# Kernel tuning notes

Measured on AMD Instinct MI355X. Metric: run time of the kernel, lower is better.

The kernel has to match this reference:

```python
import jax, jax.numpy as jnp
import numpy as np

D_MODEL = 1024
N_HEADS = 16  # long-term branch; short/medium use N_HEADS // 2


def _band_bias(seq_len, scale_factor):
    # Intended semantics of create_temporal_mask: position i may attend to
    # positions j >= i - scale_factor (recent past + all future); positions
    # further than scale_factor in the past are blocked.
    i = jnp.arange(seq_len)[:, None]
    j = jnp.arange(seq_len)[None, :]
    return jnp.where(j >= i - scale_factor, 0.0, -1e9).astype(jnp.float32)


def _mha(x, w_in, b_in, w_out, b_out, n_heads, bias):
    # Faithful nn.MultiheadAttention (batch_first, eval/no dropout).
    B, S, D = x.shape
    dk = D // n_heads
    qkv = x @ w_in.T + b_in                       # [B,S,3D]
    q, k, v = jnp.split(qkv, 3, axis=-1)
    def heads(t):
        return t.reshape(B, S, n_heads, dk).transpose(0, 2, 1, 3)  # [B,H,S,dk]
    q, k, v = heads(q), heads(k), heads(v)
    scores = jnp.einsum('bhid,bhjd->bhij', q, k) / np.sqrt(dk).astype(np.float32)
    if bias is not None:
        scores = scores + bias
    attn = jax.nn.softmax(scores, axis=-1)        # [B,H,S,S]
    out = jnp.einsum('bhij,bhjd->bhid', attn, v)  # [B,H,S,dk]
    out = out.transpose(0, 2, 1, 3).reshape(B, S, D)
    return out @ w_out.T + b_out, attn


def _layernorm(x, gamma, beta, eps=1e-5):
    mu = jnp.mean(x, axis=-1, keepdims=True)
    var = jnp.var(x, axis=-1, keepdims=True)
    return (x - mu) * jax.lax.rsqrt(var + eps) * gamma + beta


def setup_inputs() -> dict:
    key = jax.random.key(0)
    ks = jax.random.split(key, 12)
    D = D_MODEL
    s = 0.02
    inp = {
        'x': jax.random.normal(ks[0], (2, 2048, D), dtype=jnp.float32),
        'w_in_s': jax.random.normal(ks[1], (3 * D, D), dtype=jnp.float32) * s,
        'b_in_s': jnp.zeros((3 * D,), dtype=jnp.float32),
        'wo_s': jax.random.normal(ks[2], (D, D), dtype=jnp.float32) * s,
        'bo_s': jnp.zeros((D,), dtype=jnp.float32),
        'w_in_m': jax.random.normal(ks[3], (3 * D, D), dtype=jnp.float32) * s,
        'b_in_m': jnp.zeros((3 * D,), dtype=jnp.float32),
        'wo_m': jax.random.normal(ks[4], (D, D), dtype=jnp.float32) * s,
        'bo_m': jnp.zeros((D,), dtype=jnp.float32),
        'w_in_l': jax.random.normal(ks[5], (3 * D, D), dtype=jnp.float32) * s,
        'b_in_l': jnp.zeros((3 * D,), dtype=jnp.float32),
        'wo_l': jax.random.normal(ks[6], (D, D), dtype=jnp.float32) * s,
        'bo_l': jnp.zeros((D,), dtype=jnp.float32),
        'w_comb': jax.random.normal(ks[7], (D, 3 * D), dtype=jnp.float32) * s,
        'b_comb': jnp.zeros((D,), dtype=jnp.float32),
        'gamma': jnp.ones((D,), dtype=jnp.float32),
        'beta': jnp.zeros((D,), dtype=jnp.float32),
    }
    return inp


def reference(x, w_in_s, b_in_s, wo_s, bo_s,
              w_in_m, b_in_m, wo_m, bo_m,
              w_in_l, b_in_l, wo_l, bo_l,
              w_comb, b_comb, gamma, beta):
    B, S, D = x.shape
    short_bias = _band_bias(S, 10)
    medium_bias = _band_bias(S, 30)
    short_out, _ = _mha(x, w_in_s, b_in_s, wo_s, bo_s, N_HEADS // 2, short_bias)
    medium_out, _ = _mha(x, w_in_m, b_in_m, wo_m, bo_m, N_HEADS // 2, medium_bias)
    long_out, attn = _mha(x, w_in_l, b_in_l, wo_l, bo_l, N_HEADS, None)
    attn_weights = jnp.mean(attn, axis=1)  # torch default average_attn_weights=True -> [B,S,S]
    combined = jnp.concatenate([short_out, medium_out, long_out], axis=-1)
    output = combined @ w_comb.T + b_comb
    return _layernorm(output + x, gamma, beta), attn_weights
```

## Files before the change

kernel.cpp:

```cpp
#include <hip/hip_runtime.h>
#include <hip/hip_bf16.h>
#include <math.h>

#define B_ 2
#define S_ 2048
#define D_ 1024
#define M_ (B_*S_)
#define CTXLD 3072

typedef _Float16 half8_t __attribute__((ext_vector_type(8)));
typedef _Float16 half4_t __attribute__((ext_vector_type(4)));
typedef float    f32x4  __attribute__((ext_vector_type(4)));

#define GL2LDS(g, l) __builtin_amdgcn_global_load_lds( \
    (const __attribute__((address_space(1))) void*)(uintptr_t)(g), \
    (__attribute__((address_space(3))) void*)(l), 16, 0, 0)

struct GemmBatch {
    const _Float16* A;
    const _Float16* W;
    const float*    bias;
    void*           C;
    void*           C2;
};

template<int MODE>
__global__ __launch_bounds__(256) void gemm_f16(
    GemmBatch b0, GemmBatch b1, GemmBatch b2, int lda, int ldw, int ldc, int K)
{
    __shared__ __align__(16) _Float16 As[2*128*32];
    __shared__ __align__(16) _Float16 Bs[2*128*32];

    const GemmBatch G = (blockIdx.z == 0) ? b0 : ((blockIdx.z == 1) ? b1 : b2);

    const int t = threadIdx.x, lane = t & 63, w = t >> 6;
    const int bm = blockIdx.x * 128, bn = blockIdx.y * 128;
    const int wm = (w >> 1) * 64, wn = (w & 1) * 64;
    const int fr = lane & 15, q8 = (lane >> 4) * 8;
    const int srow = lane >> 2, scol = (lane & 3) * 8;

    f32x4 acc[4][4] = {};

    const _Float16* Ab = G.A + (size_t)(bm + w*32 + srow) * lda + scol;
    const _Float16* Wb = G.W + (size_t)(bn + w*32 + srow) * ldw + scol;

    for (int k0 = 0; k0 < K; k0 += 64) {
        __syncthreads();
        #pragma unroll
        for (int kc = 0; kc < 2; kc++)
            #pragma unroll
            for (int ii = 0; ii < 2; ii++) {
                GL2LDS(Ab + (size_t)(ii*16)*lda + k0 + kc*32,
                       As + kc*4096 + w*1024 + ii*512);
                GL2LDS(Wb + (size_t)(ii*16)*ldw + k0 + kc*32,
                       Bs + kc*4096 + w*1024 + ii*512);
            }
        __syncthreads();
        #pragma unroll
        for (int kc = 0; kc < 2; kc++) {
            half8_t af[4], bf[4];
            #pragma unroll
            for (int mt = 0; mt < 4; mt++)
                af[mt] = *(const half8_t*)&As[kc*4096 + (wm + mt*16 + fr)*32 + q8];
            #pragma unroll
            for (int nt = 0; nt < 4; nt++)
                bf[nt] = *(const half8_t*)&Bs[kc*4096 + (wn + nt*16 + fr)*32 + q8];
            #pragma unroll
            for (int mt = 0; mt < 4; mt++)
                #pragma unroll
                for (int nt = 0; nt < 4; nt++)
                    acc[mt][nt] = __builtin_amdgcn_mfma_f32_16x16x32_f16(
                        af[mt], bf[nt], acc[mt][nt], 0, 0, 0);
        }
    }

    const int cl = lane & 15;
    const int rq = (lane >> 4) * 4;

    if (MODE == 2 && bn >= 2048) {
        #pragma unroll
        for (int mt = 0; mt < 4; mt++) {
            int row0 = bm + wm + mt*16 + rq;
            #pragma unroll
            for (int nt = 0; nt < 4; nt++) {
                int gcol = bn + wn + nt*16 + cl;
                float bv = G.bias[gcol];
                half4_t hv = {(_Float16)(acc[mt][nt][0] + bv),
                              (_Float16)(acc[mt][nt][1] + bv),
                              (_Float16)(acc[mt][nt][2] + bv),
                              (_Float16)(acc[mt][nt][3] + bv)};
                *(half4_t*)((_Float16*)G.C2 + (size_t)(gcol - 2048) * M_ + row0) = hv;
            }
        }
        return;
    }

    #pragma unroll
    for (int mt = 0; mt < 4; mt++) {
        #pragma unroll
        for (int r = 0; r < 4; r++) {
            size_t grow = (size_t)(bm + wm + mt*16 + rq + r);
            #pragma unroll
            for (int nt = 0; nt < 4; nt++) {
                int gcol = bn + wn + nt*16 + cl;
                float v = acc[mt][nt][r] + ((MODE == 3) ? 0.f : G.bias[gcol]);
                if (MODE == 0)
                    ((float*)G.C)[grow * ldc + gcol] = v;
                else
                    ((_Float16*)G.C)[grow * ldc + gcol] = (_Float16)v;
            }
        }
    }
}

struct CastArgs {
    const float* s[5];
    _Float16*    d[5];
    int          nb[5];
};

__global__ __launch_bounds__(256) void cast_all(CastArgs a)
{
    int off = blockIdx.x;
    int seg = 0;
    while (seg < 4 && off >= a.nb[seg]) { off -= a.nb[seg]; seg++; }
    int i = off * 256 + threadIdx.x;
    float4 v = ((const float4*)a.s[seg])[i];
    half4_t h = {(_Float16)v.x, (_Float16)v.y, (_Float16)v.z, (_Float16)v.w};
    ((half4_t*)a.d[seg])[i] = h;
}

__global__ __launch_bounds__(256) void transpose_cast_wo(
    const float* s0, const float* s1, const float* s2,
    _Float16* d0, _Float16* d1, _Float16* d2)
{
    __shared__ float T[64][68];
    const float* src = blockIdx.z == 0 ? s0 : (blockIdx.z == 1 ? s1 : s2);
    _Float16*    dst = blockIdx.z == 0 ? d0 : (blockIdx.z == 1 ? d1 : d2);
    const int db = blockIdx.x * 64;
    const int eb = blockIdx.y * 64;
    const int r = threadIdx.x >> 4;
    const int c = (threadIdx.x & 15) * 4;

    #pragma unroll
    for (int rr = 0; rr < 4; rr++) {
        float4 v = *(const float4*)&src[(size_t)(db + rr*16 + r)*1024 + eb + c];
        T[rr*16 + r][c+0] = v.x; T[rr*16 + r][c+1] = v.y;
        T[rr*16 + r][c+2] = v.z; T[rr*16 + r][c+3] = v.w;
    }
    __syncthreads();
    #pragma unroll
    for (int rr = 0; rr < 4; rr++) {
        int e = rr*16 + r;
        half4_t hv = {(_Float16)T[c+0][e], (_Float16)T[c+1][e],
                      (_Float16)T[c+2][e], (_Float16)T[c+3][e]};
        *(half4_t*)&dst[(size_t)(eb + e)*1024 + db + c] = hv;
    }
}

__global__ __launch_bounds__(256) void beff_kernel(
    const float* __restrict__ w_comb, const float* __restrict__ b_comb,
    const float* __restrict__ bo_s, const float* __restrict__ bo_m,
    const float* __restrict__ bo_l, float* __restrict__ beff)
{
    __shared__ float red[4];
    const int n = blockIdx.x, t = threadIdx.x;
    float s = 0.f;
    for (int d = t; d < 1024; d += 256)
        s += w_comb[(size_t)n*3072 + d]        * bo_s[d]
           + w_comb[(size_t)n*3072 + 1024 + d] * bo_m[d]
           + w_comb[(size_t)n*3072 + 2048 + d] * bo_l[d];
    #pragma unroll
    for (int m = 32; m >= 1; m >>= 1) s += __shfl_xor(s, m);
    if ((t & 63) == 0) red[t >> 6] = s;
    __syncthreads();
    if (t == 0) beff[n] = b_comb[n] + red[0] + red[1] + red[2] + red[3];
}

template<int DK, int H, int NBR, bool LOUT>
__global__ __launch_bounds__(256, 4) void flash3(
    const _Float16* __restrict__ qk0, const _Float16* __restrict__ qk1,
    const _Float16* __restrict__ vT0, const _Float16* __restrict__ vT1,
    _Float16* __restrict__ ctx0, _Float16* __restrict__ ctx1,
    float* __restrict__ lout, int win0, int win1)
{
    constexpr int KS  = DK / 32;
    constexpr int DT  = DK / 16;
    constexpr int LDP = 40;

    __shared__ __align__(16) _Float16 Ks[KS * 64 * 32];
    __shared__ __align__(16) _Float16 Vs[2 * DK * 32];
    __shared__ __align__(16) _Float16 Ps[4 * 16 * LDP];
    __shared__ float Lw[64];

    const int t = threadIdx.x, lane = t & 63, w = t >> 6;
    const int fr = lane & 15, g = lane >> 4, k8 = g * 8;
    const int blkQ = blockIdx.x * 64;
    const int qlo  = blkQ + w * 16;
    const int h    = blockIdx.y;

    int br, b;
    if (NBR == 2) { br = blockIdx.z >> 1; b = blockIdx.z & 1; }
    else          { br = 0;               b = blockIdx.z;     }

    const _Float16* qk = br ? qk1 : qk0;
    const _Float16* vT = br ? vT1 : vT0;
    _Float16*      ctx = br ? ctx1 : ctx0;
    const int   window = br ? win1 : win0;

    const float sc = ((DK == 128) ? 0.08838834764831845f : 0.125f) * 1.44269504f;

    _Float16* PsW = Ps + w * 16 * LDP;
    const int srow = lane >> 2;
    const int scol = (lane & 3) * 8;

    half8_t qf[KS];
    #pragma unroll
    for (int kk = 0; kk < KS; kk++)
        qf[kk] = *(const half8_t*)&qk[(size_t)(b*S_ + qlo + fr)*2048 + h*DK + kk*32 + k8];

    f32x4 O[DT] = {};
    float lsum = 0.f;

    for (int j0 = 0; j0 < S_; j0 += 64) {
        if (window >= 0 && j0 + 63 < blkQ - window) continue;
        __syncthreads();

        #pragma unroll
        for (int kk = 0; kk < KS; kk++)
            GL2LDS(&qk[(size_t)(b*S_ + j0 + w*16 + srow)*2048 + 1024 + h*DK + kk*32 + scol],
                   &Ks[kk*2048 + w*512]);
        #pragma unroll
        for (int jc = 0; jc < 2; jc++)
            #pragma unroll
            for (int ii = 0; ii < DK/64; ii++)
                GL2LDS(&vT[(size_t)(h*DK + w*(DK/4) + ii*16 + srow)*M_
                           + b*S_ + j0 + jc*32 + scol],
                       &Vs[jc*DK*32 + w*(DK/4)*32 + ii*512]);
        __syncthreads();

        f32x4 st[4];
        #pragma unroll
        for (int jt = 0; jt < 4; jt++) {
            f32x4 s = {};
            #pragma unroll
            for (int kk = 0; kk < KS; kk++) {
                half8_t kf = *(const half8_t*)&Ks[kk*2048 + (jt*16 + fr)*32 + k8];
                s = __builtin_amdgcn_mfma_f32_16x16x32_f16(kf, qf[kk], s, 0, 0, 0);
            }
            st[jt] = s;
        }

        const bool full = (window < 0) || (j0 >= qlo + 15 - window);
        #pragma unroll
        for (int kc = 0; kc < 2; kc++) {
            #pragma unroll
            for (int jh = 0; jh < 2; jh++) {
                int jt = kc*2 + jh;
                float p[4];
                #pragma unroll
                for (int r = 0; r < 4; r++) {
                    float pv = exp2f(st[jt][r] * sc);
                    if (!full) {
                        int jg = j0 + jt*16 + g*4 + r;
                        if (jg < (qlo + fr) - window) pv = 0.f;
                    }
                    p[r] = pv;
                    lsum += pv;
                }
                half4_t ph = {(_Float16)p[0], (_Float16)p[1],
                              (_Float16)p[2], (_Float16)p[3]};
                *(half4_t*)&PsW[fr*LDP + jh*16 + g*4] = ph;
            }
            half8_t pf = *(const half8_t*)&PsW[fr*LDP + k8];
            #pragma unroll
            for (int dt = 0; dt < DT; dt++) {
                half8_t vf = *(const half8_t*)&Vs[kc*DK*32 + (dt*16 + fr)*32 + k8];
                O[dt] = __builtin_amdgcn_mfma_f32_16x16x32_f16(pf, vf, O[dt], 0, 0, 0);
            }
        }
    }

    lsum += __shfl_xor(lsum, 16);
    lsum += __shfl_xor(lsum, 32);
    if (g == 0) Lw[w*16 + fr] = lsum;
    float linv[4];
    #pragma unroll
    for (int r = 0; r < 4; r++)
        linv[r] = 1.f / Lw[w*16 + g*4 + r];

    if (LOUT && g == 0)
        lout[(size_t)(b*H + h)*S_ + qlo + fr] = lsum;

    #pragma unroll
    for (int r = 0; r < 4; r++) {
        _Float16* cp = ctx + (size_t)(b*S_ + qlo + g*4 + r)*CTXLD + h*DK;
        #pragma unroll
        for (int dt = 0; dt < DT; dt++)
            cp[dt*16 + fr] = (_Float16)(O[dt][r] * linv[r]);
    }
}

__global__ __launch_bounds__(256, 4) void attn_mean3(
    const _Float16* __restrict__ qk,
    const float* __restrict__ lbuf,
    float* __restrict__ attn)
{
    __shared__ __align__(16) _Float16 Ks[2 * 2 * 128 * 32];

    const int t = threadIdx.x, lane = t & 63, w = t >> 6;
    const int fr = lane & 15, g = lane >> 4, k8 = g * 8;
    const int j0 = blockIdx.x * 128;
    const int irow = blockIdx.y * 64 + w * 16;
    const int b = blockIdx.z;
    const float c1 = 0.125f * 1.44269504f;
    const int srow = lane >> 2, scol = (lane & 3) * 8;

    f32x4 acc[8] = {};

    for (int hp = 0; hp < 16; hp += 2) {
        __syncthreads();
        #pragma unroll
        for (int hh = 0; hh < 2; hh++)
            #pragma unroll
            for (int kk = 0; kk < 2; kk++)
                #pragma unroll
                for (int ii = 0; ii < 2; ii++)
                    GL2LDS(&qk[(size_t)(b*S_ + j0 + w*32 + ii*16 + srow)*2048
                               + 1024 + (hp+hh)*64 + kk*32 + scol],
                           &Ks[hh*8192 + kk*4096 + w*1024 + ii*512]);
        __syncthreads();

        #pragma unroll
        for (int hh = 0; hh < 2; hh++) {
            const int h = hp + hh;
            half8_t af[2];
            #pragma unroll
            for (int kk = 0; kk < 2; kk++)
                af[kk] = *(const half8_t*)
                    &qk[(size_t)(b*S_ + irow + fr)*2048 + h*64 + kk*32 + k8];

            float lg[4];
            #pragma unroll
            for (int r = 0; r < 4; r++)
                lg[r] = __log2f(lbuf[(size_t)(b*16 + h)*S_ + irow + g*4 + r]) + 4.0f;

            #pragma unroll
            for (int nt = 0; nt < 8; nt++) {
                f32x4 s = {};
                #pragma unroll
                for (int kk = 0; kk < 2; kk++) {
                    half8_t bf = *(const half8_t*)
                        &Ks[hh*8192 + kk*4096 + (nt*16 + fr)*32 + k8];
                    s = __builtin_amdgcn_mfma_f32_16x16x32_f16(af[kk], bf, s, 0, 0, 0);
                }
                #pragma unroll
                for (int r = 0; r < 4; r++)
                    acc[nt][r] += exp2f(s[r] * c1 - lg[r]);
            }
        }
    }

    #pragma unroll
    for (int r = 0; r < 4; r++) {
        float* p = attn + (size_t)(b*S_ + irow + g*4 + r)*S_ + j0;
        #pragma unroll
        for (int nt = 0; nt < 8; nt++)
            p[nt*16 + fr] = acc[nt][r];
    }
}

__global__ __launch_bounds__(256) void ln_residual(
    const float* __restrict__ pre, const float* __restrict__ x,
    const float* __restrict__ gamma, const float* __restrict__ beta,
    float* __restrict__ out)
{
    __shared__ float redS[4], redQ[4];
    const int row = blockIdx.x;
    const int t = threadIdx.x;
    size_t base = (size_t)row * D_ + t * 4;

    float4 v  = *(const float4*)(pre + base);
    float4 xv = *(const float4*)(x + base);
    v.x += xv.x; v.y += xv.y; v.z += xv.z; v.w += xv.w;

    float s = v.x + v.y + v.z + v.w;
    float q = v.x*v.x + v.y*v.y + v.z*v.z + v.w*v.w;
    #pragma unroll
    for (int m = 32; m >= 1; m >>= 1) {
        s += __shfl_xor(s, m);
        q += __shfl_xor(q, m);
    }
    int wave = t >> 6;
    if ((t & 63) == 0) { redS[wave] = s; redQ[wave] = q; }
    __syncthreads();
    s = redS[0] + redS[1] + redS[2] + redS[3];
    q = redQ[0] + redQ[1] + redQ[2] + redQ[3];

    float mean = s * (1.f / D_);
    float var  = q * (1.f / D_) - mean * mean;
    float rstd = rsqrtf(var + 1e-5f);

    float4 g  = *(const float4*)(gamma + t * 4);
    float4 be = *(const float4*)(beta + t * 4);
    float4 o;
    o.x = (v.x - mean) * rstd * g.x + be.x;
    o.y = (v.y - mean) * rstd * g.y + be.y;
    o.z = (v.z - mean) * rstd * g.z + be.z;
    o.w = (v.w - mean) * rstd * g.w + be.w;
    *(float4*)(out + base) = o;
}

extern "C" void kernel_launch(void* const* d_in, const int* in_sizes, int n_in,
                              void* d_out, int out_size, void* d_ws, size_t ws_size,
                              hipStream_t stream)
{
    (void)in_sizes; (void)n_in; (void)out_size; (void)ws_size;
    const float* x      = (const float*)d_in[0];
    const float* w_in_s = (const float*)d_in[1];
    const float* b_in_s = (const float*)d_in[2];
    const float* wo_s   = (const float*)d_in[3];
    const float* bo_s   = (const float*)d_in[4];
    const float* w_in_m = (const float*)d_in[5];
    const float* b_in_m = (const float*)d_in[6];
    const float* wo_m   = (const float*)d_in[7];
    const float* bo_m   = (const float*)d_in[8];
    const float* w_in_l = (const float*)d_in[9];
    const float* b_in_l = (const float*)d_in[10];
    const float* wo_l   = (const float*)d_in[11];
    const float* bo_l   = (const float*)d_in[12];
    const float* w_comb = (const float*)d_in[13];
    const float* b_comb = (const float*)d_in[14];
    const float* gamma  = (const float*)d_in[15];
    const float* beta   = (const float*)d_in[16];

    float* out    = (float*)d_out;
    float* attn_o = out + (size_t)M_ * D_;

    char* W = (char*)d_ws;
    _Float16* qk_s   = (_Float16*)(W);
    _Float16* qk_m   = (_Float16*)(W + 16777216);
    _Float16* vT_s   = (_Float16*)(W + 33554432);
    _Float16* vT_m   = (_Float16*)(W + 41943040);
    _Float16* ctxall = (_Float16*)(W + 50331648);
    float*    lbuf   = (float*)   (W + 75497472);
    _Float16* x_h    = (_Float16*)(W + 75759616);
    _Float16* wpool  = (_Float16*)(W + 84148224);
    float*    beff   = (float*)   (W + 121896960);
    _Float16* qk_l   = qk_s;
    _Float16* vT_l   = vT_s;
    float*    pre    = (float*)qk_m;

    _Float16* w_in_s_h = wpool;
    _Float16* w_in_m_h = wpool + 3145728;
    _Float16* w_in_l_h = wpool + 6291456;
    _Float16* w_comb_h = wpool + 9437184;
    _Float16* woT_s    = wpool + 12582912;
    _Float16* woT_m    = wpool + 13631488;
    _Float16* woT_l    = wpool + 14680064;
    _Float16* weff     = wpool + 15728640;

    dim3 blk(256);
    GemmBatch nil = { nullptr, nullptr, nullptr, nullptr, nullptr };

    CastArgs ca;
    ca.s[0]=x;      ca.d[0]=x_h;      ca.nb[0]=4096;
    ca.s[1]=w_in_s; ca.d[1]=w_in_s_h; ca.nb[1]=3072;
    ca.s[2]=w_in_m; ca.d[2]=w_in_m_h; ca.nb[2]=3072;
    ca.s[3]=w_in_l; ca.d[3]=w_in_l_h; ca.nb[3]=3072;
    ca.s[4]=w_comb; ca.d[4]=w_comb_h; ca.nb[4]=3072;
    cast_all<<<dim3(16384), blk, 0, stream>>>(ca);

    transpose_cast_wo<<<dim3(16, 16, 3), blk, 0, stream>>>(
        wo_s, wo_m, wo_l, woT_s, woT_m, woT_l);

    GemmBatch we0 = { w_comb_h + 0,    woT_s, nullptr, weff + 0,    nullptr };
    GemmBatch we1 = { w_comb_h + 1024, woT_m, nullptr, weff + 1024, nullptr };
    GemmBatch we2 = { w_comb_h + 2048, woT_l, nullptr, weff + 2048, nullptr };
    gemm_f16<3><<<dim3(8, 8, 3), blk, 0, stream>>>(we0, we1, we2, 3072, 1024, 3072, 1024);

    beff_kernel<<<dim3(1024), blk, 0, stream>>>(w_comb, b_comb, bo_s, bo_m, bo_l, beff);

    GemmBatch qs = { x_h, w_in_s_h, b_in_s, qk_s, vT_s };
    GemmBatch qm = { x_h, w_in_m_h, b_in_m, qk_m, vT_m };
    gemm_f16<2><<<dim3(M_/128, 3072/128, 2), blk, 0, stream>>>(qs, qm, nil, D_, D_, 2048, D_);

    flash3<128, 8, 2, false><<<dim3(S_/64, 8, 4), blk, 0, stream>>>(
        qk_s, qk_m, vT_s, vT_m, ctxall + 0, ctxall + 1024, nullptr, 10, 30);

    GemmBatch ql = { x_h, w_in_l_h, b_in_l, qk_l, vT_l };
    gemm_f16<2><<<dim3(M_/128, 3072/128, 1), blk, 0, stream>>>(ql, nil, nil, D_, D_, 2048, D_);

    flash3<64, 16, 1, true><<<dim3(S_/64, 16, 2), blk, 0, stream>>>(
        qk_l, qk_l, vT_l, vT_l, ctxall + 2048, ctxall + 2048, lbuf, -1, -1);

    attn_mean3<<<dim3(S_/128, S_/64, B_), blk, 0, stream>>>(qk_l, lbuf, attn_o);

    GemmBatch fb = { ctxall, weff, beff, pre, nullptr };
    gemm_f16<0><<<dim3(M_/128, D_/128, 1), blk, 0, stream>>>(fb, nil, nil, 3072, 3072, D_, 3072);

    ln_residual<<<dim3(M_), blk, 0, stream>>>(pre, x, gamma, beta, out);
}
```

Before: 632.3 us.

## Merge all three QKV GEMMs and flash attentions into single batched launches

The workspace is re-laid out so the short, medium and long branches each get separate QKV buffers, which lets one batched GEMM launch produce all three projections. A single flash_mega kernel then runs the long-branch full attention, now with a 128-wide key tile, together with the short and medium banded attention. The banded blocks are issued in reverse query order to help balance load. The aim is to cut launches and inter-kernel tail gaps and to fill the GPU better, at the cost of more LDS per block and higher workspace usage. vT_l now aliases the w_comb_h region, which is assumed free after weff is computed.

```diff
diff --git a/kernel.cpp b/kernel.cpp
--- a/kernel.cpp
+++ b/kernel.cpp
@@ -177,36 +177,27 @@
     if (t == 0) beff[n] = b_comb[n] + red[0] + red[1] + red[2] + red[3];
 }
 
-template<int DK, int H, int NBR, bool LOUT>
-__global__ __launch_bounds__(256, 4) void flash3(
-    const _Float16* __restrict__ qk0, const _Float16* __restrict__ qk1,
-    const _Float16* __restrict__ vT0, const _Float16* __restrict__ vT1,
-    _Float16* __restrict__ ctx0, _Float16* __restrict__ ctx1,
-    float* __restrict__ lout, int win0, int win1)
+template<int DK, int BJ, bool LOUT>
+__device__ __forceinline__ void flash_body(
+    _Float16* lds, float* Lw,
+    const _Float16* __restrict__ qk, const _Float16* __restrict__ vT,
+    _Float16* __restrict__ ctx, float* __restrict__ lout,
+    int window, int b, int h, int qblk, int H)
 {
     constexpr int KS  = DK / 32;
     constexpr int DT  = DK / 16;
+    constexpr int JT  = BJ / 16;
+    constexpr int JC  = BJ / 32;
     constexpr int LDP = 40;
 
-    __shared__ __align__(16) _Float16 Ks[KS * 64 * 32];
-    __shared__ __align__(16) _Float16 Vs[2 * DK * 32];
-    __shared__ __align__(16) _Float16 Ps[4 * 16 * LDP];
-    __shared__ float Lw[64];
+    _Float16* Ks = lds;
+    _Float16* Vs = lds + DK*BJ;
+    _Float16* Ps = lds + 2*DK*BJ;
 
     const int t = threadIdx.x, lane = t & 63, w = t >> 6;
     const int fr = lane & 15, g = lane >> 4, k8 = g * 8;
-    const int blkQ = blockIdx.x * 64;
+    const int blkQ = qblk * 64;
     const int qlo  = blkQ + w * 16;
-    const int h    = blockIdx.y;
-
-    int br, b;
-    if (NBR == 2) { br = blockIdx.z >> 1; b = blockIdx.z & 1; }
-    else          { br = 0;               b = blockIdx.z;     }
-
-    const _Float16* qk = br ? qk1 : qk0;
-    const _Float16* vT = br ? vT1 : vT0;
-    _Float16*      ctx = br ? ctx1 : ctx0;
-    const int   window = br ? win1 : win0;
 
     const float sc = ((DK == 128) ? 0.08838834764831845f : 0.125f) * 1.44269504f;
 
@@ -222,16 +213,19 @@
     f32x4 O[DT] = {};
     float lsum = 0.f;
 
-    for (int j0 = 0; j0 < S_; j0 += 64) {
-        if (window >= 0 && j0 + 63 < blkQ - window) continue;
+    for (int j0 = 0; j0 < S_; j0 += BJ) {
+        if (window >= 0 && j0 + BJ - 1 < blkQ - window) continue;
         __syncthreads();
 
         #pragma unroll
         for (int kk = 0; kk < KS; kk++)
-            GL2LDS(&qk[(size_t)(b*S_ + j0 + w*16 + srow)*2048 + 1024 + h*DK + kk*32 + scol],
-                   &Ks[kk*2048 + w*512]);
-        #pragma unroll
-        for (int jc = 0; jc < 2; jc++)
+            #pragma unroll
+            for (int ii = 0; ii < BJ/64; ii++)
+                GL2LDS(&qk[(size_t)(b*S_ + j0 + w*(BJ/4) + ii*16 + srow)*2048
+                           + 1024 + h*DK + kk*32 + scol],
+                       &Ks[kk*BJ*32 + w*(BJ/4)*32 + ii*512]);
+        #pragma unroll
+        for (int jc = 0; jc < JC; jc++)
             #pragma unroll
             for (int ii = 0; ii < DK/64; ii++)
                 GL2LDS(&vT[(size_t)(h*DK + w*(DK/4) + ii*16 + srow)*M_
@@ -239,13 +233,13 @@
                        &Vs[jc*DK*32 + w*(DK/4)*32 + ii*512]);
         __syncthreads();
 
-        f32x4 st[4];
-        #pragma unroll
-        for (int jt = 0; jt < 4; jt++) {
+        f32x4 st[JT];
+        #pragma unroll
+        for (int jt = 0; jt < JT; jt++) {
             f32x4 s = {};
             #pragma unroll
             for (int kk = 0; kk < KS; kk++) {
-                half8_t kf = *(const half8_t*)&Ks[kk*2048 + (jt*16 + fr)*32 + k8];
+                half8_t kf = *(const half8_t*)&Ks[kk*BJ*32 + (jt*16 + fr)*32 + k8];
                 s = __builtin_amdgcn_mfma_f32_16x16x32_f16(kf, qf[kk], s, 0, 0, 0);
             }
             st[jt] = s;
@@ -253,7 +247,7 @@
 
         const bool full = (window < 0) || (j0 >= qlo + 15 - window);
         #pragma unroll
-        for (int kc = 0; kc < 2; kc++) {
+        for (int kc = 0; kc < JC; kc++) {
             #pragma unroll
             for (int jh = 0; jh < 2; jh++) {
                 int jt = kc*2 + jh;
@@ -298,6 +292,33 @@
         #pragma unroll
         for (int dt = 0; dt < DT; dt++)
             cp[dt*16 + fr] = (_Float16)(O[dt][r] * linv[r]);
+    }
+}
+
+__global__ __launch_bounds__(256, 4) void flash_mega(
+    const _Float16* __restrict__ qk_s, const _Float16* __restrict__ qk_m,
+    const _Float16* __restrict__ qk_l,
+    const _Float16* __restrict__ vT_s, const _Float16* __restrict__ vT_m,
+    const _Float16* __restrict__ vT_l,
+    _Float16* __restrict__ ctxall, float* __restrict__ lbuf)
+{
+    __shared__ __align__(16) _Float16 lds[18944];
+    __shared__ float Lw[64];
+
+    const int bid = blockIdx.x;
+    if (bid < 1024) {
+        int qblk = bid & 31, h = (bid >> 5) & 15, b = bid >> 9;
+        flash_body<64, 128, true>(lds, Lw, qk_l, vT_l, ctxall + 2048, lbuf,
+                                  -1, b, h, qblk, 16);
+    } else {
+        int r = bid - 1024;
+        int qblk = 31 - (r & 31);
+        int h = (r >> 5) & 7;
+        int z = r >> 8;
+        int br = z >> 1, b = z & 1;
+        flash_body<128, 64, false>(lds, Lw, br ? qk_m : qk_s, br ? vT_m : vT_s,
+                                   ctxall + (br ? 1024 : 0), nullptr,
+                                   br ? 30 : 10, b, h, qblk, 8);
     }
 }
 
@@ -438,27 +459,25 @@
     float* attn_o = out + (size_t)M_ * D_;
 
     char* W = (char*)d_ws;
-    _Float16* qk_s   = (_Float16*)(W);
-    _Float16* qk_m   = (_Float16*)(W + 16777216);
-    _Float16* vT_s   = (_Float16*)(W + 33554432);
-    _Float16* vT_m   = (_Float16*)(W + 41943040);
-    _Float16* ctxall = (_Float16*)(W + 50331648);
-    float*    lbuf   = (float*)   (W + 75497472);
-    _Float16* x_h    = (_Float16*)(W + 75759616);
-    _Float16* wpool  = (_Float16*)(W + 84148224);
-    float*    beff   = (float*)   (W + 121896960);
-    _Float16* qk_l   = qk_s;
-    _Float16* vT_l   = vT_s;
-    float*    pre    = (float*)qk_m;
-
-    _Float16* w_in_s_h = wpool;
-    _Float16* w_in_m_h = wpool + 3145728;
-    _Float16* w_in_l_h = wpool + 6291456;
-    _Float16* w_comb_h = wpool + 9437184;
-    _Float16* woT_s    = wpool + 12582912;
-    _Float16* woT_m    = wpool + 13631488;
-    _Float16* woT_l    = wpool + 14680064;
-    _Float16* weff     = wpool + 15728640;
+    _Float16* w_in_s_h = (_Float16*)(W);
+    _Float16* w_in_m_h = (_Float16*)(W + 6291456);
+    _Float16* w_in_l_h = (_Float16*)(W + 12582912);
+    _Float16* w_comb_h = (_Float16*)(W + 18874368);
+    _Float16* woT_s    = (_Float16*)(W + 25165824);
+    _Float16* woT_m    = (_Float16*)(W + 27262976);
+    _Float16* woT_l    = (_Float16*)(W + 29360128);
+    _Float16* weff     = (_Float16*)(W + 31457280);
+    _Float16* qk_s     = (_Float16*)(W + 37748736);
+    _Float16* qk_m     = (_Float16*)(W + 54525952);
+    _Float16* qk_l     = (_Float16*)(W + 71303168);
+    _Float16* vT_s     = (_Float16*)(W + 88080384);
+    _Float16* vT_m     = (_Float16*)(W + 96468992);
+    _Float16* ctxall   = (_Float16*)(W + 104857600);
+    _Float16* x_h      = (_Float16*)(W + 130023424);
+    float*    lbuf     = (float*)   (W + 138412032);
+    float*    beff     = (float*)   (W + 138674432);
+    _Float16* vT_l     = w_comb_h;
+    float*    pre      = (float*)qk_m;
 
     dim3 blk(256);
     GemmBatch nil = { nullptr, nullptr, nullptr, nullptr, nullptr };
@@ -483,16 +502,11 @@
 
     GemmBatch qs = { x_h, w_in_s_h, b_in_s, qk_s, vT_s };
     GemmBatch qm = { x_h, w_in_m_h, b_in_m, qk_m, vT_m };
-    gemm_f16<2><<<dim3(M_/128, 3072/128, 2), blk, 0, stream>>>(qs, qm, nil, D_, D_, 2048, D_);
-
-    flash3<128, 8, 2, false><<<dim3(S_/64, 8, 4), blk, 0, stream>>>(
-        qk_s, qk_m, vT_s, vT_m, ctxall + 0, ctxall + 1024, nullptr, 10, 30);
-
     GemmBatch ql = { x_h, w_in_l_h, b_in_l, qk_l, vT_l };
-    gemm_f16<2><<<dim3(M_/128, 3072/128, 1), blk, 0, stream>>>(ql, nil, nil, D_, D_, 2048, D_);
-
-    flash3<64, 16, 1, true><<<dim3(S_/64, 16, 2), blk, 0, stream>>>(
-        qk_l, qk_l, vT_l, vT_l, ctxall + 2048, ctxall + 2048, lbuf, -1, -1);
+    gemm_f16<2><<<dim3(M_/128, 3072/128, 3), blk, 0, stream>>>(qs, qm, ql, D_, D_, 2048, D_);
+
+    flash_mega<<<dim3(2048), blk, 0, stream>>>(
+        qk_s, qk_m, qk_l, vT_s, vT_m, vT_l, ctxall, lbuf);
 
     attn_mean3<<<dim3(S_/128, S_/64, B_), blk, 0, stream>>>(qk_l, lbuf, attn_o);
 
```

Measured after the change: 609.7 us. -3.6%, faster.
